# Optimization experiments

Measured on AMD Instinct MI355X. Metric: run time of the kernel, lower is better.

Reference implementation:

```python
import jax, jax.numpy as jnp
import numpy as np
import math

B, S, D, DFF = 32, 2048, 512, 512


def setup_inputs() -> dict:
    key = jax.random.key(0)
    ks = jax.random.split(key, 10)
    s = 1.0 / math.sqrt(D)
    inp = {
        "x": jax.random.normal(ks[0], (B, S, D), dtype=jnp.float32),
        "Wq": jax.random.uniform(ks[1], (DFF, D), jnp.float32, -s, s),
        "bq": jax.random.uniform(ks[2], (DFF,), jnp.float32, -s, s),
        "Wk": jax.random.uniform(ks[3], (DFF, D), jnp.float32, -s, s),
        "bk": jax.random.uniform(ks[4], (DFF,), jnp.float32, -s, s),
        "Wv": jax.random.uniform(ks[5], (DFF, D), jnp.float32, -s, s),
        "bv": jax.random.uniform(ks[6], (DFF,), jnp.float32, -s, s),
        "Wt": jax.random.uniform(ks[7], (1, S), jnp.float32, -1.0 / math.sqrt(S), 1.0 / math.sqrt(S)),
        "bt": jax.random.uniform(ks[8], (1,), jnp.float32, -1.0 / math.sqrt(S), 1.0 / math.sqrt(S)),
    }
    return inp


def reference(x, Wq, bq, Wk, bk, Wv, bv, Wt, bt):
    # QKV projections: [B,S,DFF]
    q = jnp.einsum('bsd,fd->bsf', x, Wq) + bq
    k = jnp.einsum('bsd,fd->bsf', x, Wk) + bk
    v = jnp.einsum('bsd,fd->bsf', x, Wv) + bv
    # attention scores: [B,S,S]
    scores = jnp.einsum('bsf,btf->bst', q, k) / math.sqrt(DFF)
    # temporal reduction Linear(S->1): [B,S,1] -> [B,S]
    ta = jnp.einsum('bst,t->bs', scores, Wt[0]) + bt[0]
    # V-weighted sum: [B,DFF]
    latent = jnp.einsum('bsf,bs->bf', v, ta)
    return latent
```

## Files before the change

### kernel.cpp

```cpp
#include <hip/hip_runtime.h>

#define NB 32
#define NS 2048
#define ND 512
#define NFF 512
#define SCALE 0.044194173824159216f

#define CPB 64
#define ROWS 32

__device__ __forceinline__ float dot4(float4 a, float4 b) {
    return a.x * b.x + a.y * b.y + a.z * b.z + a.w * b.w;
}

__device__ __forceinline__ float wave_reduce(float p) {
#pragma unroll
    for (int m = 1; m < 64; m <<= 1) p += __shfl_xor(p, m, 64);
    return p;
}

__global__ void __launch_bounds__(256) k_xw(const float* __restrict__ x,
                                            const float* __restrict__ Wt,
                                            float* __restrict__ xwp,
                                            float* __restrict__ wqs,
                                            float* __restrict__ cb2) {
    const int b = blockIdx.x >> 6;
    const int chunk = blockIdx.x & 63;
    const int s0 = chunk * ROWS;
    const int t = threadIdx.x;
    const int col = t & 127;
    const int half = t >> 7;

    if (blockIdx.x < NB) {
        const int bz = blockIdx.x;
        wqs[bz * ND + t] = 0.f;
        wqs[bz * ND + 256 + t] = 0.f;
        if (t == 0) cb2[bz] = 0.f;
    }

    const float4* xb = (const float4*)(x + (size_t)b * NS * ND);
    float4 acc = make_float4(0.f, 0.f, 0.f, 0.f);
#pragma unroll 4
    for (int i = 0; i < 16; i++) {
        int s = s0 + half + 2 * i;
        float w = Wt[s];
        float4 v = xb[(size_t)s * 128 + col];
        acc.x += w * v.x; acc.y += w * v.y; acc.z += w * v.z; acc.w += w * v.w;
    }
    __shared__ float4 red[128];
    if (half == 1) red[col] = acc;
    __syncthreads();
    if (half == 0) {
        float4 o = red[col];
        o.x += acc.x; o.y += acc.y; o.z += acc.z; o.w += acc.w;
        ((float4*)xwp)[(size_t)blockIdx.x * 128 + col] = o;
    }
}

__global__ void __launch_bounds__(256) k_kw(const float* __restrict__ xwp,
                                            const float* __restrict__ Wt,
                                            const float* __restrict__ Wk,
                                            const float* __restrict__ bk,
                                            const float* __restrict__ Wq,
                                            const float* __restrict__ bq,
                                            const float* __restrict__ bt,
                                            float* __restrict__ wqs,
                                            float* __restrict__ cb2) {
    const int b = blockIdx.x >> 3;
    const int f0 = (blockIdx.x & 7) * 64;
    const int t = threadIdx.x;
    const int wv = t >> 6;
    const int lane = t & 63;
    __shared__ float sA[ND];
    __shared__ float kfl[64];
    __shared__ float sW[4];
    __shared__ float swt_s;
    {
        float a0 = 0.f, a1 = 0.f;
        const float* p = xwp + (size_t)b * CPB * ND + t;
#pragma unroll 8
        for (int c = 0; c < CPB; c++) {
            a0 += p[(size_t)c * ND];
            a1 += p[(size_t)c * ND + 256];
        }
        sA[t] = a0;
        sA[256 + t] = a1;
    }
    if (wv == 0) {
        float a = 0.f;
#pragma unroll
        for (int j = 0; j < 32; j++) a += Wt[j * 64 + lane];
        a = wave_reduce(a);
        if (lane == 0) swt_s = a;
    }
    __syncthreads();
    {
        const float4* xw4 = (const float4*)sA;
        const float4 xa = xw4[lane];
        const float4 xc = xw4[64 + lane];
        const float sw = swt_s;
        float cbp = 0.f;
#pragma unroll 4
        for (int j = 0; j < 16; j++) {
            int f = f0 + wv * 16 + j;
            const float4* wr = (const float4*)(Wk + (size_t)f * ND);
            float pd = dot4(xa, wr[lane]) + dot4(xc, wr[64 + lane]);
            pd = wave_reduce(pd);
            if (lane == 0) {
                float kfs = SCALE * (pd + bk[f] * sw);
                kfl[wv * 16 + j] = kfs;
                cbp += kfs * bq[f];
            }
        }
        if (lane == 0) sW[wv] = cbp;
    }
    __syncthreads();
    {
        float a0 = 0.f, a1 = 0.f;
#pragma unroll 8
        for (int j = 0; j < 64; j++) {
            float kf = kfl[j];
            const float* wr = Wq + (size_t)(f0 + j) * ND;
            a0 += kf * wr[t];
            a1 += kf * wr[256 + t];
        }
        atomicAdd(&wqs[b * ND + t], a0);
        atomicAdd(&wqs[b * ND + 256 + t], a1);
        if (t == 0) {
            float c = sW[0] + sW[1] + sW[2] + sW[3];
            if ((blockIdx.x & 7) == 0) c += bt[0];
            atomicAdd(&cb2[b], c);
        }
    }
}

__global__ void __launch_bounds__(256) k_ta_xt(const float* __restrict__ x,
                                               const float* __restrict__ wqs,
                                               const float* __restrict__ cb2,
                                               float* __restrict__ xtp,
                                               float* __restrict__ stp) {
    const int b = blockIdx.x >> 6;
    const int chunk = blockIdx.x & 63;
    const int wv = threadIdx.x >> 6;
    const int lane = threadIdx.x & 63;
    const float4* xb = (const float4*)(x + (size_t)b * NS * ND);
    const float4* wq4 = (const float4*)(wqs + b * ND);
    const float4 w0 = wq4[lane];
    const float4 w1 = wq4[64 + lane];
    const float c = cb2[b];
    float4 a0 = make_float4(0.f, 0.f, 0.f, 0.f);
    float4 a1 = make_float4(0.f, 0.f, 0.f, 0.f);
    float sta = 0.f;
#pragma unroll 2
    for (int i = 0; i < 8; i++) {
        int s = chunk * ROWS + wv * 8 + i;
        float4 v0 = xb[(size_t)s * 128 + lane];
        float4 v1 = xb[(size_t)s * 128 + 64 + lane];
        float pd = dot4(v0, w0) + dot4(v1, w1);
        pd = wave_reduce(pd);
        float ta = pd + c;
        a0.x += ta * v0.x; a0.y += ta * v0.y; a0.z += ta * v0.z; a0.w += ta * v0.w;
        a1.x += ta * v1.x; a1.y += ta * v1.y; a1.z += ta * v1.z; a1.w += ta * v1.w;
        sta += ta;
    }
    __shared__ float4 sh0[4][64];
    __shared__ float4 sh1[4][64];
    __shared__ float sW[4];
    sh0[wv][lane] = a0;
    sh1[wv][lane] = a1;
    if (lane == 0) sW[wv] = sta;
    __syncthreads();
    const int t = threadIdx.x;
    float4* dst = (float4*)xtp + (size_t)blockIdx.x * 128;
    if (t < 64) {
        float4 s0 = sh0[0][t], s1 = sh0[1][t], s2 = sh0[2][t], s3 = sh0[3][t];
        dst[t] = make_float4(s0.x + s1.x + s2.x + s3.x,
                             s0.y + s1.y + s2.y + s3.y,
                             s0.z + s1.z + s2.z + s3.z,
                             s0.w + s1.w + s2.w + s3.w);
    } else if (t < 128) {
        int l = t - 64;
        float4 s0 = sh1[0][l], s1 = sh1[1][l], s2 = sh1[2][l], s3 = sh1[3][l];
        dst[64 + l] = make_float4(s0.x + s1.x + s2.x + s3.x,
                                  s0.y + s1.y + s2.y + s3.y,
                                  s0.z + s1.z + s2.z + s3.z,
                                  s0.w + s1.w + s2.w + s3.w);
    } else if (t == 128) {
        stp[blockIdx.x] = sW[0] + sW[1] + sW[2] + sW[3];
    }
}

__global__ void __launch_bounds__(256) k_latent(const float* __restrict__ xtp,
                                                const float* __restrict__ stp,
                                                const float* __restrict__ Wv,
                                                const float* __restrict__ bv,
                                                float* __restrict__ out) {
    const int b = blockIdx.x >> 3;
    const int f0 = (blockIdx.x & 7) * 64;
    const int t = threadIdx.x;
    const int wv = t >> 6;
    const int lane = t & 63;
    __shared__ float sA[ND];
    __shared__ float sts;
    {
        float a0 = 0.f, a1 = 0.f;
        const float* p = xtp + (size_t)b * CPB * ND + t;
#pragma unroll 8
        for (int c = 0; c < CPB; c++) {
            a0 += p[(size_t)c * ND];
            a1 += p[(size_t)c * ND + 256];
        }
        sA[t] = a0;
        sA[256 + t] = a1;
        if (t == 0) {
            float s = 0.f;
            const float* sp = stp + b * CPB;
#pragma unroll
            for (int c = 0; c < CPB; c++) s += sp[c];
            sts = s;
        }
    }
    __syncthreads();
    const float4* xt4 = (const float4*)sA;
    const float4 xa = xt4[lane];
    const float4 xc = xt4[64 + lane];
    const float stb = sts;
#pragma unroll 4
    for (int j = 0; j < 16; j++) {
        int f = f0 + wv * 16 + j;
        const float4* wr = (const float4*)(Wv + (size_t)f * ND);
        float pd = dot4(xa, wr[lane]) + dot4(xc, wr[64 + lane]);
        pd = wave_reduce(pd);
        if (lane == 0) out[b * NFF + f] = pd + bv[f] * stb;
    }
}

extern "C" void kernel_launch(void* const* d_in, const int* in_sizes, int n_in,
                              void* d_out, int out_size, void* d_ws, size_t ws_size,
                              hipStream_t stream) {
    const float* x  = (const float*)d_in[0];
    const float* Wq = (const float*)d_in[1];
    const float* bq = (const float*)d_in[2];
    const float* Wk = (const float*)d_in[3];
    const float* bk = (const float*)d_in[4];
    const float* Wv = (const float*)d_in[5];
    const float* bv = (const float*)d_in[6];
    const float* Wt = (const float*)d_in[7];
    const float* bt = (const float*)d_in[8];
    float* out = (float*)d_out;

    float* w = (float*)d_ws;
    float* xwp  = w;
    float* xtp  = w + 1048576;
    float* stp  = w + 2097152;
    float* wqs  = w + 2099200;
    float* cb2  = w + 2115584;

    k_xw<<<NB * CPB, 256, 0, stream>>>(x, Wt, xwp, wqs, cb2);
    k_kw<<<256, 256, 0, stream>>>(xwp, Wt, Wk, bk, Wq, bq, bt, wqs, cb2);
    k_ta_xt<<<NB * CPB, 256, 0, stream>>>(x, wqs, cb2, xtp, stp);
    k_latent<<<256, 256, 0, stream>>>(xtp, stp, Wv, bv, out);
}
```

Measured before the change: 268.6 us.

## Split weight stages into more kernels, batch shuffle reductions, accumulate xt with atomics

The small middle stage is split into separate kernels: a reduction of the per-chunk xw partials, a K-weight GEMV over 512 blocks, and a Wq transpose-GEMV with no atomics. In the main streaming pass, all 8 row loads are issued up front and their 8 wave reductions are interleaved, to expose memory-level parallelism and hide shuffle latency. The per-chunk xt partial buffer is replaced by float atomicAdds into a per-batch accumulator, which removes the partial-reduction loop from the final kernel. This adds two kernel launches and atomic contention, and raises register pressure from the 8 buffered float4 pairs.

Result: slower. 284.2 us (+5.8%).

```diff
diff --git a/kernel.cpp b/kernel.cpp
--- a/kernel.cpp
+++ b/kernel.cpp
@@ -22,8 +22,8 @@
 __global__ void __launch_bounds__(256) k_xw(const float* __restrict__ x,
                                             const float* __restrict__ Wt,
                                             float* __restrict__ xwp,
-                                            float* __restrict__ wqs,
-                                            float* __restrict__ cb2) {
+                                            float* __restrict__ xt,
+                                            float* __restrict__ st) {
     const int b = blockIdx.x >> 6;
     const int chunk = blockIdx.x & 63;
     const int s0 = chunk * ROWS;
@@ -33,9 +33,9 @@
 
     if (blockIdx.x < NB) {
         const int bz = blockIdx.x;
-        wqs[bz * ND + t] = 0.f;
-        wqs[bz * ND + 256 + t] = 0.f;
-        if (t == 0) cb2[bz] = 0.f;
+        xt[bz * ND + t] = 0.f;
+        xt[bz * ND + 256 + t] = 0.f;
+        if (t == 0) st[bz] = 0.f;
     }
 
     const float4* xb = (const float4*)(x + (size_t)b * NS * ND);
@@ -57,88 +57,92 @@
     }
 }
 
-__global__ void __launch_bounds__(256) k_kw(const float* __restrict__ xwp,
-                                            const float* __restrict__ Wt,
+__global__ void __launch_bounds__(256) k_xwred(const float* __restrict__ xwp,
+                                               const float* __restrict__ Wt,
+                                               float* __restrict__ xw,
+                                               float* __restrict__ sw) {
+    const int b = blockIdx.x >> 1;
+    const int d0 = (blockIdx.x & 1) * 256;
+    const int t = threadIdx.x;
+    const float* p = xwp + (size_t)b * CPB * ND + d0 + t;
+    float a = 0.f;
+#pragma unroll 8
+    for (int c = 0; c < CPB; c++) a += p[(size_t)c * ND];
+    xw[b * ND + d0 + t] = a;
+    if (blockIdx.x == 0 && t < 64) {
+        float s = 0.f;
+#pragma unroll
+        for (int i = 0; i < 32; i++) s += Wt[t + 64 * i];
+        s = wave_reduce(s);
+        if (t == 0) sw[0] = s;
+    }
+}
+
+__global__ void __launch_bounds__(256) k_kw(const float* __restrict__ xw,
                                             const float* __restrict__ Wk,
                                             const float* __restrict__ bk,
-                                            const float* __restrict__ Wq,
-                                            const float* __restrict__ bq,
-                                            const float* __restrict__ bt,
-                                            float* __restrict__ wqs,
-                                            float* __restrict__ cb2) {
-    const int b = blockIdx.x >> 3;
-    const int f0 = (blockIdx.x & 7) * 64;
+                                            const float* __restrict__ sw,
+                                            float* __restrict__ kwS) {
+    const int b = blockIdx.x >> 4;
+    const int f0 = (blockIdx.x & 15) * 32;
     const int t = threadIdx.x;
     const int wv = t >> 6;
     const int lane = t & 63;
-    __shared__ float sA[ND];
-    __shared__ float kfl[64];
-    __shared__ float sW[4];
-    __shared__ float swt_s;
-    {
-        float a0 = 0.f, a1 = 0.f;
-        const float* p = xwp + (size_t)b * CPB * ND + t;
-#pragma unroll 8
-        for (int c = 0; c < CPB; c++) {
-            a0 += p[(size_t)c * ND];
-            a1 += p[(size_t)c * ND + 256];
+    const float4* xw4 = (const float4*)(xw + b * ND);
+    const float4 xa = xw4[lane];
+    const float4 xc = xw4[64 + lane];
+    const float sws = sw[0];
+#pragma unroll
+    for (int j = 0; j < 8; j++) {
+        int f = f0 + wv * 8 + j;
+        const float4* wr = (const float4*)(Wk + (size_t)f * ND);
+        float pd = dot4(xa, wr[lane]) + dot4(xc, wr[64 + lane]);
+        pd = wave_reduce(pd);
+        if (lane == 0) kwS[b * NFF + f] = SCALE * (pd + bk[f] * sws);
+    }
+}
+
+__global__ void __launch_bounds__(256) k_wqs(const float* __restrict__ kwS,
+                                             const float* __restrict__ Wq,
+                                             const float* __restrict__ bq,
+                                             const float* __restrict__ bt,
+                                             float* __restrict__ wqs,
+                                             float* __restrict__ cb2) {
+    const int b = blockIdx.x >> 1;
+    const int d0 = (blockIdx.x & 1) * 256;
+    const int t = threadIdx.x;
+    __shared__ float sk[NFF];
+    __shared__ float red[256];
+    sk[t] = kwS[b * NFF + t];
+    sk[256 + t] = kwS[b * NFF + 256 + t];
+    __syncthreads();
+    const float* wp = Wq + d0 + t;
+    float a0 = 0.f, a1 = 0.f, a2 = 0.f, a3 = 0.f;
+#pragma unroll 4
+    for (int f = 0; f < NFF; f += 4) {
+        a0 += sk[f]     * wp[(size_t)f * ND];
+        a1 += sk[f + 1] * wp[(size_t)(f + 1) * ND];
+        a2 += sk[f + 2] * wp[(size_t)(f + 2) * ND];
+        a3 += sk[f + 3] * wp[(size_t)(f + 3) * ND];
+    }
+    wqs[b * ND + d0 + t] = (a0 + a1) + (a2 + a3);
+    if ((blockIdx.x & 1) == 0) {
+        float v = sk[t] * bq[t] + sk[256 + t] * bq[256 + t];
+        red[t] = v;
+        __syncthreads();
+        for (int off = 128; off > 0; off >>= 1) {
+            if (t < off) red[t] += red[t + off];
+            __syncthreads();
         }
-        sA[t] = a0;
-        sA[256 + t] = a1;
-    }
-    if (wv == 0) {
-        float a = 0.f;
-#pragma unroll
-        for (int j = 0; j < 32; j++) a += Wt[j * 64 + lane];
-        a = wave_reduce(a);
-        if (lane == 0) swt_s = a;
-    }
-    __syncthreads();
-    {
-        const float4* xw4 = (const float4*)sA;
-        const float4 xa = xw4[lane];
-        const float4 xc = xw4[64 + lane];
-        const float sw = swt_s;
-        float cbp = 0.f;
-#pragma unroll 4
-        for (int j = 0; j < 16; j++) {
-            int f = f0 + wv * 16 + j;
-            const float4* wr = (const float4*)(Wk + (size_t)f * ND);
-            float pd = dot4(xa, wr[lane]) + dot4(xc, wr[64 + lane]);
-            pd = wave_reduce(pd);
-            if (lane == 0) {
-                float kfs = SCALE * (pd + bk[f] * sw);
-                kfl[wv * 16 + j] = kfs;
-                cbp += kfs * bq[f];
-            }
-        }
-        if (lane == 0) sW[wv] = cbp;
-    }
-    __syncthreads();
-    {
-        float a0 = 0.f, a1 = 0.f;
-#pragma unroll 8
-        for (int j = 0; j < 64; j++) {
-            float kf = kfl[j];
-            const float* wr = Wq + (size_t)(f0 + j) * ND;
-            a0 += kf * wr[t];
-            a1 += kf * wr[256 + t];
-        }
-        atomicAdd(&wqs[b * ND + t], a0);
-        atomicAdd(&wqs[b * ND + 256 + t], a1);
-        if (t == 0) {
-            float c = sW[0] + sW[1] + sW[2] + sW[3];
-            if ((blockIdx.x & 7) == 0) c += bt[0];
-            atomicAdd(&cb2[b], c);
-        }
+        if (t == 0) cb2[b] = red[0] + bt[0];
     }
 }
 
 __global__ void __launch_bounds__(256) k_ta_xt(const float* __restrict__ x,
                                                const float* __restrict__ wqs,
                                                const float* __restrict__ cb2,
-                                               float* __restrict__ xtp,
-                                               float* __restrict__ stp) {
+                                               float* __restrict__ xt,
+                                               float* __restrict__ st) {
     const int b = blockIdx.x >> 6;
     const int chunk = blockIdx.x & 63;
     const int wv = threadIdx.x >> 6;
@@ -148,19 +152,29 @@
     const float4 w0 = wq4[lane];
     const float4 w1 = wq4[64 + lane];
     const float c = cb2[b];
+
+    float4 v0[8], v1[8];
+    float pd[8];
+#pragma unroll
+    for (int i = 0; i < 8; i++) {
+        int s = chunk * ROWS + wv * 8 + i;
+        v0[i] = xb[(size_t)s * 128 + lane];
+        v1[i] = xb[(size_t)s * 128 + 64 + lane];
+        pd[i] = dot4(v0[i], w0) + dot4(v1[i], w1);
+    }
+#pragma unroll
+    for (int m = 1; m < 64; m <<= 1) {
+#pragma unroll
+        for (int i = 0; i < 8; i++) pd[i] += __shfl_xor(pd[i], m, 64);
+    }
     float4 a0 = make_float4(0.f, 0.f, 0.f, 0.f);
     float4 a1 = make_float4(0.f, 0.f, 0.f, 0.f);
     float sta = 0.f;
-#pragma unroll 2
+#pragma unroll
     for (int i = 0; i < 8; i++) {
-        int s = chunk * ROWS + wv * 8 + i;
-        float4 v0 = xb[(size_t)s * 128 + lane];
-        float4 v1 = xb[(size_t)s * 128 + 64 + lane];
-        float pd = dot4(v0, w0) + dot4(v1, w1);
-        pd = wave_reduce(pd);
-        float ta = pd + c;
-        a0.x += ta * v0.x; a0.y += ta * v0.y; a0.z += ta * v0.z; a0.w += ta * v0.w;
-        a1.x += ta * v1.x; a1.y += ta * v1.y; a1.z += ta * v1.z; a1.w += ta * v1.w;
+        float ta = pd[i] + c;
+        a0.x += ta * v0[i].x; a0.y += ta * v0[i].y; a0.z += ta * v0[i].z; a0.w += ta * v0[i].w;
+        a1.x += ta * v1[i].x; a1.y += ta * v1[i].y; a1.z += ta * v1[i].z; a1.w += ta * v1[i].w;
         sta += ta;
     }
     __shared__ float4 sh0[4][64];
@@ -171,63 +185,42 @@
     if (lane == 0) sW[wv] = sta;
     __syncthreads();
     const int t = threadIdx.x;
-    float4* dst = (float4*)xtp + (size_t)blockIdx.x * 128;
+    float* xbt = xt + b * ND;
     if (t < 64) {
         float4 s0 = sh0[0][t], s1 = sh0[1][t], s2 = sh0[2][t], s3 = sh0[3][t];
-        dst[t] = make_float4(s0.x + s1.x + s2.x + s3.x,
-                             s0.y + s1.y + s2.y + s3.y,
-                             s0.z + s1.z + s2.z + s3.z,
-                             s0.w + s1.w + s2.w + s3.w);
+        atomicAdd(&xbt[4 * t + 0], s0.x + s1.x + s2.x + s3.x);
+        atomicAdd(&xbt[4 * t + 1], s0.y + s1.y + s2.y + s3.y);
+        atomicAdd(&xbt[4 * t + 2], s0.z + s1.z + s2.z + s3.z);
+        atomicAdd(&xbt[4 * t + 3], s0.w + s1.w + s2.w + s3.w);
     } else if (t < 128) {
         int l = t - 64;
         float4 s0 = sh1[0][l], s1 = sh1[1][l], s2 = sh1[2][l], s3 = sh1[3][l];
-        dst[64 + l] = make_float4(s0.x + s1.x + s2.x + s3.x,
-                                  s0.y + s1.y + s2.y + s3.y,
-                                  s0.z + s1.z + s2.z + s3.z,
-                                  s0.w + s1.w + s2.w + s3.w);
+        atomicAdd(&xbt[256 + 4 * l + 0], s0.x + s1.x + s2.x + s3.x);
+        atomicAdd(&xbt[256 + 4 * l + 1], s0.y + s1.y + s2.y + s3.y);
+        atomicAdd(&xbt[256 + 4 * l + 2], s0.z + s1.z + s2.z + s3.z);
+        atomicAdd(&xbt[256 + 4 * l + 3], s0.w + s1.w + s2.w + s3.w);
     } else if (t == 128) {
-        stp[blockIdx.x] = sW[0] + sW[1] + sW[2] + sW[3];
-    }
-}
-
-__global__ void __launch_bounds__(256) k_latent(const float* __restrict__ xtp,
-                                                const float* __restrict__ stp,
-                                                const float* __restrict__ Wv,
-                                                const float* __restrict__ bv,
-                                                float* __restrict__ out) {
-    const int b = blockIdx.x >> 3;
-    const int f0 = (blockIdx.x & 7) * 64;
+        atomicAdd(&st[b], sW[0] + sW[1] + sW[2] + sW[3]);
+    }
+}
+
+__global__ void __launch_bounds__(256) k_out(const float* __restrict__ xt,
+                                             const float* __restrict__ st,
+                                             const float* __restrict__ Wv,
+                                             const float* __restrict__ bv,
+                                             float* __restrict__ out) {
+    const int b = blockIdx.x >> 4;
+    const int f0 = (blockIdx.x & 15) * 32;
     const int t = threadIdx.x;
     const int wv = t >> 6;
     const int lane = t & 63;
-    __shared__ float sA[ND];
-    __shared__ float sts;
-    {
-        float a0 = 0.f, a1 = 0.f;
-        const float* p = xtp + (size_t)b * CPB * ND + t;
-#pragma unroll 8
-        for (int c = 0; c < CPB; c++) {
-            a0 += p[(size_t)c * ND];
-            a1 += p[(size_t)c * ND + 256];
-        }
-        sA[t] = a0;
-        sA[256 + t] = a1;
-        if (t == 0) {
-            float s = 0.f;
-            const float* sp = stp + b * CPB;
-#pragma unroll
-            for (int c = 0; c < CPB; c++) s += sp[c];
-            sts = s;
-        }
-    }
-    __syncthreads();
-    const float4* xt4 = (const float4*)sA;
+    const float4* xt4 = (const float4*)(xt + b * ND);
     const float4 xa = xt4[lane];
     const float4 xc = xt4[64 + lane];
-    const float stb = sts;
-#pragma unroll 4
-    for (int j = 0; j < 16; j++) {
-        int f = f0 + wv * 16 + j;
+    const float stb = st[b];
+#pragma unroll
+    for (int j = 0; j < 8; j++) {
+        int f = f0 + wv * 8 + j;
         const float4* wr = (const float4*)(Wv + (size_t)f * ND);
         float pd = dot4(xa, wr[lane]) + dot4(xc, wr[64 + lane]);
         pd = wave_reduce(pd);
@@ -250,14 +243,19 @@
     float* out = (float*)d_out;
 
     float* w = (float*)d_ws;
-    float* xwp  = w;
-    float* xtp  = w + 1048576;
-    float* stp  = w + 2097152;
-    float* wqs  = w + 2099200;
-    float* cb2  = w + 2115584;
-
-    k_xw<<<NB * CPB, 256, 0, stream>>>(x, Wt, xwp, wqs, cb2);
-    k_kw<<<256, 256, 0, stream>>>(xwp, Wt, Wk, bk, Wq, bq, bt, wqs, cb2);
-    k_ta_xt<<<NB * CPB, 256, 0, stream>>>(x, wqs, cb2, xtp, stp);
-    k_latent<<<256, 256, 0, stream>>>(xtp, stp, Wv, bv, out);
-}
+    float* xwp = w;
+    float* xw  = w + 1048576;
+    float* kwS = w + 1064960;
+    float* wqs = w + 1081344;
+    float* cb2 = w + 1097728;
+    float* xt  = w + 1097760;
+    float* st  = w + 1114144;
+    float* sw  = w + 1114176;
+
+    k_xw<<<NB * CPB, 256, 0, stream>>>(x, Wt, xwp, xt, st);
+    k_xwred<<<64, 256, 0, stream>>>(xwp, Wt, xw, sw);
+    k_kw<<<512, 256, 0, stream>>>(xw, Wk, bk, sw, kwS);
+    k_wqs<<<64, 256, 0, stream>>>(kwS, Wq, bq, bt, wqs, cb2);
+    k_ta_xt<<<NB * CPB, 256, 0, stream>>>(x, wqs, cb2, xt, st);
+    k_out<<<512, 256, 0, stream>>>(xt, st, Wv, bv, out);
+}
```

## Use one 1024-thread block per batch for middle kernels, drop atomics, batch reductions

Applied to the files above, without the earlier changes.

The two small middle kernels (k_kw, k_latent) are remapped from eight 256-thread blocks per batch to one 1024-thread block per batch. Partial sums are combined in shared memory and written directly, so the global atomics and the zero-init in k_xw go away. Wave shuffle reductions are batched four or eight at a time for more instruction-level parallelism, and k_ta_xt issues all its row loads before reducing. The catch is only 32 blocks on a many-CU GPU, so each batch's Wk/Wq/Wv traffic is served by a single CU.

After: 278.8 us. +3.8%, slower.

```diff
diff --git a/kernel.cpp b/kernel.cpp
--- a/kernel.cpp
+++ b/kernel.cpp
@@ -5,7 +5,6 @@
 #define ND 512
 #define NFF 512
 #define SCALE 0.044194173824159216f
-
 #define CPB 64
 #define ROWS 32
 
@@ -19,24 +18,25 @@
     return p;
 }
 
+__device__ __forceinline__ void reduce4(float& p0, float& p1, float& p2, float& p3) {
+#pragma unroll
+    for (int m = 1; m < 64; m <<= 1) {
+        p0 += __shfl_xor(p0, m, 64);
+        p1 += __shfl_xor(p1, m, 64);
+        p2 += __shfl_xor(p2, m, 64);
+        p3 += __shfl_xor(p3, m, 64);
+    }
+}
+
 __global__ void __launch_bounds__(256) k_xw(const float* __restrict__ x,
                                             const float* __restrict__ Wt,
-                                            float* __restrict__ xwp,
-                                            float* __restrict__ wqs,
-                                            float* __restrict__ cb2) {
+                                            float* __restrict__ xwp) {
     const int b = blockIdx.x >> 6;
     const int chunk = blockIdx.x & 63;
     const int s0 = chunk * ROWS;
     const int t = threadIdx.x;
     const int col = t & 127;
     const int half = t >> 7;
-
-    if (blockIdx.x < NB) {
-        const int bz = blockIdx.x;
-        wqs[bz * ND + t] = 0.f;
-        wqs[bz * ND + 256 + t] = 0.f;
-        if (t == 0) cb2[bz] = 0.f;
-    }
 
     const float4* xb = (const float4*)(x + (size_t)b * NS * ND);
     float4 acc = make_float4(0.f, 0.f, 0.f, 0.f);
@@ -57,80 +57,109 @@
     }
 }
 
-__global__ void __launch_bounds__(256) k_kw(const float* __restrict__ xwp,
-                                            const float* __restrict__ Wt,
-                                            const float* __restrict__ Wk,
-                                            const float* __restrict__ bk,
-                                            const float* __restrict__ Wq,
-                                            const float* __restrict__ bq,
-                                            const float* __restrict__ bt,
-                                            float* __restrict__ wqs,
-                                            float* __restrict__ cb2) {
-    const int b = blockIdx.x >> 3;
-    const int f0 = (blockIdx.x & 7) * 64;
+__global__ void __launch_bounds__(1024, 1)
+k_mid(const float* __restrict__ xwp, const float* __restrict__ Wt,
+      const float* __restrict__ Wk, const float* __restrict__ bk,
+      const float* __restrict__ Wq, const float* __restrict__ bq,
+      const float* __restrict__ bt, float* __restrict__ wqs,
+      float* __restrict__ cb2) {
+    const int b = blockIdx.x;
     const int t = threadIdx.x;
+    const int c4 = t & 127;
+    const int grp = t >> 7;
+    __shared__ __align__(16) float4 tmp4[1024];
+    __shared__ __align__(16) float sxw[ND];
+    __shared__ float skw[NFF];
+    __shared__ float sW[16];
+    __shared__ float ssw;
+
+    {
+        const float4* xp = (const float4*)(xwp + (size_t)b * CPB * ND) + c4;
+        float4 a = make_float4(0.f, 0.f, 0.f, 0.f);
+#pragma unroll
+        for (int c = 0; c < 8; c++) {
+            float4 v = xp[(size_t)(grp * 8 + c) * 128];
+            a.x += v.x; a.y += v.y; a.z += v.z; a.w += v.w;
+        }
+        tmp4[t] = a;
+    }
+    if (t < 64) {
+        float s = 0.f;
+#pragma unroll
+        for (int i = 0; i < 32; i++) s += Wt[t + 64 * i];
+        s = wave_reduce(s);
+        if (t == 0) ssw = s;
+    }
+    __syncthreads();
+    if (t < 128) {
+        float4 a = tmp4[t];
+#pragma unroll
+        for (int g = 1; g < 8; g++) {
+            float4 v = tmp4[g * 128 + t];
+            a.x += v.x; a.y += v.y; a.z += v.z; a.w += v.w;
+        }
+        ((float4*)sxw)[t] = a;
+    }
+    __syncthreads();
+
     const int wv = t >> 6;
     const int lane = t & 63;
-    __shared__ float sA[ND];
-    __shared__ float kfl[64];
-    __shared__ float sW[4];
-    __shared__ float swt_s;
+    const float sw = ssw;
+    const float4 xa = ((const float4*)sxw)[lane];
+    const float4 xc = ((const float4*)sxw)[64 + lane];
+    float cbp = 0.f;
+#pragma unroll
+    for (int j = 0; j < 8; j++) {
+        const int f = wv * 32 + j * 4;
+        const float4* r0 = (const float4*)(Wk + (size_t)f * ND);
+        const float4* r1 = (const float4*)(Wk + (size_t)(f + 1) * ND);
+        const float4* r2 = (const float4*)(Wk + (size_t)(f + 2) * ND);
+        const float4* r3 = (const float4*)(Wk + (size_t)(f + 3) * ND);
+        float p0 = dot4(xa, r0[lane]) + dot4(xc, r0[64 + lane]);
+        float p1 = dot4(xa, r1[lane]) + dot4(xc, r1[64 + lane]);
+        float p2 = dot4(xa, r2[lane]) + dot4(xc, r2[64 + lane]);
+        float p3 = dot4(xa, r3[lane]) + dot4(xc, r3[64 + lane]);
+        reduce4(p0, p1, p2, p3);
+        if (lane == 0) {
+            float k0 = SCALE * (p0 + bk[f]     * sw);
+            float k1 = SCALE * (p1 + bk[f + 1] * sw);
+            float k2 = SCALE * (p2 + bk[f + 2] * sw);
+            float k3 = SCALE * (p3 + bk[f + 3] * sw);
+            skw[f] = k0; skw[f + 1] = k1; skw[f + 2] = k2; skw[f + 3] = k3;
+            cbp += k0 * bq[f] + k1 * bq[f + 1] + k2 * bq[f + 2] + k3 * bq[f + 3];
+        }
+    }
+    if (lane == 0) sW[wv] = cbp;
+    __syncthreads();
+
     {
-        float a0 = 0.f, a1 = 0.f;
-        const float* p = xwp + (size_t)b * CPB * ND + t;
-#pragma unroll 8
-        for (int c = 0; c < CPB; c++) {
-            a0 += p[(size_t)c * ND];
-            a1 += p[(size_t)c * ND + 256];
-        }
-        sA[t] = a0;
-        sA[256 + t] = a1;
-    }
-    if (wv == 0) {
-        float a = 0.f;
-#pragma unroll
-        for (int j = 0; j < 32; j++) a += Wt[j * 64 + lane];
-        a = wave_reduce(a);
-        if (lane == 0) swt_s = a;
-    }
-    __syncthreads();
-    {
-        const float4* xw4 = (const float4*)sA;
-        const float4 xa = xw4[lane];
-        const float4 xc = xw4[64 + lane];
-        const float sw = swt_s;
-        float cbp = 0.f;
+        float4 acc = make_float4(0.f, 0.f, 0.f, 0.f);
+        const float4* wq4 = (const float4*)Wq + c4;
 #pragma unroll 4
-        for (int j = 0; j < 16; j++) {
-            int f = f0 + wv * 16 + j;
-            const float4* wr = (const float4*)(Wk + (size_t)f * ND);
-            float pd = dot4(xa, wr[lane]) + dot4(xc, wr[64 + lane]);
-            pd = wave_reduce(pd);
-            if (lane == 0) {
-                float kfs = SCALE * (pd + bk[f] * sw);
-                kfl[wv * 16 + j] = kfs;
-                cbp += kfs * bq[f];
-            }
-        }
-        if (lane == 0) sW[wv] = cbp;
-    }
-    __syncthreads();
-    {
-        float a0 = 0.f, a1 = 0.f;
-#pragma unroll 8
         for (int j = 0; j < 64; j++) {
-            float kf = kfl[j];
-            const float* wr = Wq + (size_t)(f0 + j) * ND;
-            a0 += kf * wr[t];
-            a1 += kf * wr[256 + t];
-        }
-        atomicAdd(&wqs[b * ND + t], a0);
-        atomicAdd(&wqs[b * ND + 256 + t], a1);
-        if (t == 0) {
-            float c = sW[0] + sW[1] + sW[2] + sW[3];
-            if ((blockIdx.x & 7) == 0) c += bt[0];
-            atomicAdd(&cb2[b], c);
-        }
+            int f = grp * 64 + j;
+            float kf = skw[f];
+            float4 v = wq4[(size_t)f * 128];
+            acc.x += kf * v.x; acc.y += kf * v.y;
+            acc.z += kf * v.z; acc.w += kf * v.w;
+        }
+        tmp4[t] = acc;
+    }
+    __syncthreads();
+    if (t < 128) {
+        float4 a = tmp4[t];
+#pragma unroll
+        for (int g = 1; g < 8; g++) {
+            float4 v = tmp4[g * 128 + t];
+            a.x += v.x; a.y += v.y; a.z += v.z; a.w += v.w;
+        }
+        ((float4*)(wqs + b * ND))[t] = a;
+    }
+    if (t == 0) {
+        float cb = 0.f;
+#pragma unroll
+        for (int i = 0; i < 16; i++) cb += sW[i];
+        cb2[b] = cb + bt[0];
     }
 }
 
@@ -148,19 +177,29 @@
     const float4 w0 = wq4[lane];
     const float4 w1 = wq4[64 + lane];
     const float c = cb2[b];
+
+    float4 v0[8], v1[8];
+    float pd[8];
+#pragma unroll
+    for (int i = 0; i < 8; i++) {
+        int s = chunk * ROWS + wv * 8 + i;
+        v0[i] = xb[(size_t)s * 128 + lane];
+        v1[i] = xb[(size_t)s * 128 + 64 + lane];
+        pd[i] = dot4(v0[i], w0) + dot4(v1[i], w1);
+    }
+#pragma unroll
+    for (int m = 1; m < 64; m <<= 1) {
+#pragma unroll
+        for (int i = 0; i < 8; i++) pd[i] += __shfl_xor(pd[i], m, 64);
+    }
     float4 a0 = make_float4(0.f, 0.f, 0.f, 0.f);
     float4 a1 = make_float4(0.f, 0.f, 0.f, 0.f);
     float sta = 0.f;
-#pragma unroll 2
+#pragma unroll
     for (int i = 0; i < 8; i++) {
-        int s = chunk * ROWS + wv * 8 + i;
-        float4 v0 = xb[(size_t)s * 128 + lane];
-        float4 v1 = xb[(size_t)s * 128 + 64 + lane];
-        float pd = dot4(v0, w0) + dot4(v1, w1);
-        pd = wave_reduce(pd);
-        float ta = pd + c;
-        a0.x += ta * v0.x; a0.y += ta * v0.y; a0.z += ta * v0.z; a0.w += ta * v0.w;
-        a1.x += ta * v1.x; a1.y += ta * v1.y; a1.z += ta * v1.z; a1.w += ta * v1.w;
+        float ta = pd[i] + c;
+        a0.x += ta * v0[i].x; a0.y += ta * v0[i].y; a0.z += ta * v0[i].z; a0.w += ta * v0[i].w;
+        a1.x += ta * v1[i].x; a1.y += ta * v1[i].y; a1.z += ta * v1[i].z; a1.w += ta * v1[i].w;
         sta += ta;
     }
     __shared__ float4 sh0[4][64];
@@ -190,48 +229,68 @@
     }
 }
 
-__global__ void __launch_bounds__(256) k_latent(const float* __restrict__ xtp,
-                                                const float* __restrict__ stp,
-                                                const float* __restrict__ Wv,
-                                                const float* __restrict__ bv,
-                                                float* __restrict__ out) {
-    const int b = blockIdx.x >> 3;
-    const int f0 = (blockIdx.x & 7) * 64;
+__global__ void __launch_bounds__(1024, 1)
+k_fin(const float* __restrict__ xtp, const float* __restrict__ stp,
+      const float* __restrict__ Wv, const float* __restrict__ bv,
+      float* __restrict__ out) {
+    const int b = blockIdx.x;
     const int t = threadIdx.x;
+    const int c4 = t & 127;
+    const int grp = t >> 7;
+    __shared__ __align__(16) float4 tmp4[1024];
+    __shared__ __align__(16) float sxt[ND];
+    __shared__ float sst;
+
+    {
+        const float4* xp = (const float4*)(xtp + (size_t)b * CPB * ND) + c4;
+        float4 a = make_float4(0.f, 0.f, 0.f, 0.f);
+#pragma unroll
+        for (int c = 0; c < 8; c++) {
+            float4 v = xp[(size_t)(grp * 8 + c) * 128];
+            a.x += v.x; a.y += v.y; a.z += v.z; a.w += v.w;
+        }
+        tmp4[t] = a;
+    }
+    if (t < 64) {
+        float s = stp[b * CPB + t];
+        s = wave_reduce(s);
+        if (t == 0) sst = s;
+    }
+    __syncthreads();
+    if (t < 128) {
+        float4 a = tmp4[t];
+#pragma unroll
+        for (int g = 1; g < 8; g++) {
+            float4 v = tmp4[g * 128 + t];
+            a.x += v.x; a.y += v.y; a.z += v.z; a.w += v.w;
+        }
+        ((float4*)sxt)[t] = a;
+    }
+    __syncthreads();
+
     const int wv = t >> 6;
     const int lane = t & 63;
-    __shared__ float sA[ND];
-    __shared__ float sts;
-    {
-        float a0 = 0.f, a1 = 0.f;
-        const float* p = xtp + (size_t)b * CPB * ND + t;
-#pragma unroll 8
-        for (int c = 0; c < CPB; c++) {
-            a0 += p[(size_t)c * ND];
-            a1 += p[(size_t)c * ND + 256];
-        }
-        sA[t] = a0;
-        sA[256 + t] = a1;
-        if (t == 0) {
-            float s = 0.f;
-            const float* sp = stp + b * CPB;
-#pragma unroll
-            for (int c = 0; c < CPB; c++) s += sp[c];
-            sts = s;
-        }
-    }
-    __syncthreads();
-    const float4* xt4 = (const float4*)sA;
-    const float4 xa = xt4[lane];
-    const float4 xc = xt4[64 + lane];
-    const float stb = sts;
-#pragma unroll 4
-    for (int j = 0; j < 16; j++) {
-        int f = f0 + wv * 16 + j;
-        const float4* wr = (const float4*)(Wv + (size_t)f * ND);
-        float pd = dot4(xa, wr[lane]) + dot4(xc, wr[64 + lane]);
-        pd = wave_reduce(pd);
-        if (lane == 0) out[b * NFF + f] = pd + bv[f] * stb;
+    const float4 xa = ((const float4*)sxt)[lane];
+    const float4 xc = ((const float4*)sxt)[64 + lane];
+    const float stb = sst;
+#pragma unroll
+    for (int j = 0; j < 8; j++) {
+        const int f = wv * 32 + j * 4;
+        const float4* r0 = (const float4*)(Wv + (size_t)f * ND);
+        const float4* r1 = (const float4*)(Wv + (size_t)(f + 1) * ND);
+        const float4* r2 = (const float4*)(Wv + (size_t)(f + 2) * ND);
+        const float4* r3 = (const float4*)(Wv + (size_t)(f + 3) * ND);
+        float p0 = dot4(xa, r0[lane]) + dot4(xc, r0[64 + lane]);
+        float p1 = dot4(xa, r1[lane]) + dot4(xc, r1[64 + lane]);
+        float p2 = dot4(xa, r2[lane]) + dot4(xc, r2[64 + lane]);
+        float p3 = dot4(xa, r3[lane]) + dot4(xc, r3[64 + lane]);
+        reduce4(p0, p1, p2, p3);
+        if (lane == 0) {
+            out[b * NFF + f]     = p0 + bv[f]     * stb;
+            out[b * NFF + f + 1] = p1 + bv[f + 1] * stb;
+            out[b * NFF + f + 2] = p2 + bv[f + 2] * stb;
+            out[b * NFF + f + 3] = p3 + bv[f + 3] * stb;
+        }
     }
 }
 
@@ -250,14 +309,14 @@
     float* out = (float*)d_out;
 
     float* w = (float*)d_ws;
-    float* xwp  = w;
-    float* xtp  = w + 1048576;
-    float* stp  = w + 2097152;
-    float* wqs  = w + 2099200;
-    float* cb2  = w + 2115584;
-
-    k_xw<<<NB * CPB, 256, 0, stream>>>(x, Wt, xwp, wqs, cb2);
-    k_kw<<<256, 256, 0, stream>>>(xwp, Wt, Wk, bk, Wq, bq, bt, wqs, cb2);
+    float* xwp = w;
+    float* xtp = w + 1048576;
+    float* stp = w + 2097152;
+    float* wqs = w + 2099200;
+    float* cb2 = w + 2115584;
+
+    k_xw<<<NB * CPB, 256, 0, stream>>>(x, Wt, xwp);
+    k_mid<<<NB, 1024, 0, stream>>>(xwp, Wt, Wk, bk, Wq, bq, bt, wqs, cb2);
     k_ta_xt<<<NB * CPB, 256, 0, stream>>>(x, wqs, cb2, xtp, stp);
-    k_latent<<<256, 256, 0, stream>>>(xtp, stp, Wv, bv, out);
-}
+    k_fin<<<NB, 1024, 0, stream>>>(xtp, stp, Wv, bv, out);
+}
```
